# Optimization experiments

Measured on AMD Instinct MI355X. Metric: run time of the kernel, lower is better.

The kernel has to match this reference:

```python
import jax, jax.numpy as jnp
import numpy as np

# physical constants from init_kwargs
N_ACT = 10.0                      # adaptive_activation_n (same for all layers)
MU1, MU2 = 1.0, 10.0
SIGMA = 24.5
G = 0.98
RHO1, RHO2 = 100.0, 1000.0
U_REF, L_REF = 1.0, 0.5
RHO_REF = RHO2
EPS = 2.220446049250313e-16       # np.finfo(float).eps used in abs_interface_grad
ONE_WE = SIGMA / (RHO_REF * U_REF ** 2 * L_REF)
ONE_FR = G * L_REF / U_REF ** 2
RE_DEN = RHO_REF * U_REF * L_REF


def setup_inputs() -> dict:
    key = jax.random.key(0)
    ks = jax.random.split(key, 8)
    N, H, NL = 32768, 250, 7

    def glorot(k, shape):
        fan_in, fan_out = shape[-2], shape[-1]
        s = jnp.sqrt(2.0 / (fan_in + fan_out)).astype(jnp.float32)
        return jax.random.normal(k, shape, dtype=jnp.float32) * s

    return {
        "x": jax.random.normal(ks[0], (N, 1), dtype=jnp.float32),
        "y": jax.random.normal(ks[1], (N, 1), dtype=jnp.float32),
        "t": jax.random.uniform(ks[2], (N, 1), dtype=jnp.float32),
        "W_in": glorot(ks[3], (3, H)),
        "b_in": jnp.zeros((H,), jnp.float32),
        "W_h": glorot(ks[4], (NL - 1, H, H)),
        "b_h": jnp.zeros((NL - 1, H), jnp.float32),
        "W_out": glorot(ks[5], (H, 4)),   # 4 heads: u, v, p, a
        "b_out": jnp.zeros((4,), jnp.float32),
        "act_coeff": jnp.full((NL,), 0.1, jnp.float32),  # adaptive activation coeffs
    }


def _mlp(pt, W_in, b_in, W_h, b_h, W_out, b_out, act_coeff):
    # pt: (3,) -> (4,) outputs [u, v, p=exp(z), a=sigmoid(z)]
    h = jnp.tanh(N_ACT * act_coeff[0] * (pt @ W_in + b_in))
    for i in range(W_h.shape[0]):  # structural loop over 6 hidden layers
        h = jnp.tanh(N_ACT * act_coeff[i + 1] * (h @ W_h[i] + b_h[i]))
    z = h @ W_out + b_out
    return jnp.stack([z[0], z[1], jnp.exp(z[2]), jax.nn.sigmoid(z[3])])


def _pde_residuals(x, y, t, W_in, b_in, W_h, b_h, W_out, b_out, act_coeff):
    pts = jnp.concatenate([x, y, t], axis=1)  # (N, 3)
    f = lambda p: _mlp(p, W_in, b_in, W_h, b_h, W_out, b_out, act_coeff)
    vals = jax.vmap(f)(pts)                              # (N, 4)
    jac = jax.vmap(jax.jacfwd(f))(pts)                   # (N, 4, 3)
    hess = jax.vmap(jax.jacfwd(jax.jacfwd(f)))(pts)      # (N, 4, 3, 3)

    u, v, a = vals[:, 0], vals[:, 1], vals[:, 3]
    u_x, u_y, u_t = jac[:, 0, 0], jac[:, 0, 1], jac[:, 0, 2]
    v_x, v_y, v_t = jac[:, 1, 0], jac[:, 1, 1], jac[:, 1, 2]
    p_x, p_y = jac[:, 2, 0], jac[:, 2, 1]
    a_x, a_y, a_t = jac[:, 3, 0], jac[:, 3, 1], jac[:, 3, 2]
    u_xx, u_yy = hess[:, 0, 0, 0], hess[:, 0, 1, 1]
    v_xx, v_yy = hess[:, 1, 0, 0], hess[:, 1, 1, 1]
    a_xx, a_yy, a_xy = hess[:, 3, 0, 0], hess[:, 3, 1, 1], hess[:, 3, 0, 1]

    mu = MU2 + (MU1 - MU2) * a
    mu_x = (MU1 - MU2) * a_x
    mu_y = (MU1 - MU2) * a_y
    rho = RHO2 + (RHO1 - RHO2) * a

    g = jnp.sqrt(a_x ** 2 + a_y ** 2 + EPS)
    curvature = -((a_xx + a_yy) / g
                  - (a_x ** 2 * a_xx + a_y ** 2 * a_yy + 2.0 * a_x * a_y * a_xy) / (g ** 3))

    one_Re = mu / RE_DEN
    one_Re_x = mu_x / RE_DEN
    one_Re_y = mu_y / RE_DEN

    PDE_m = u_x + v_y
    PDE_a = a_t + u * a_x + v * a_y
    PDE_u = ((u_t + u * u_x + v * u_y) * rho / RHO_REF + p_x
             - ONE_WE * curvature * a_x - one_Re * (u_xx + u_yy)
             - 2.0 * one_Re_x * u_x - one_Re_y * (u_y + v_x))
    PDE_v = ((v_t + u * v_x + v * v_y) * rho / RHO_REF + p_y
             - ONE_WE * curvature * a_y - one_Re * (v_xx + v_yy)
             - rho / RHO_REF * ONE_FR
             - 2.0 * one_Re_y * v_y - one_Re_x * (u_y + v_x))
    return jnp.stack([PDE_m, PDE_u, PDE_v, PDE_a], axis=1)  # (N, 4)


def reference(x, y, t, W_in, b_in, W_h, b_h, W_out, b_out, act_coeff):
    r = _pde_residuals(x, y, t, W_in, b_in, W_h, b_h, W_out, b_out, act_coeff)
    # match PDE_caller's tuple of (N,1) residuals
    return (r[:, 0:1], r[:, 1:2], r[:, 2:3], r[:, 3:4])
```

## Files before the change

kernel.cpp:

```cpp
#include <hip/hip_runtime.h>
#include <math.h>
#include <stdint.h>

#define HP 256
#define PTS 16
#define ROWS 128
#define PSTR 264
#define NLAYER 6
#define WT_ELEMS (6*256*256)
#define PREP_TILES 96

typedef _Float16 half8 __attribute__((ext_vector_type(8)));
typedef _Float16 half2v __attribute__((ext_vector_type(2)));
typedef float  float16v __attribute__((ext_vector_type(16)));

#define C_WI 0
#define C_BI 768
#define C_BH 1024
#define C_WO 2560
#define C_TOT 3584

__device__ __forceinline__ float fast_tanh(float x) {
    float e = __expf(2.0f * x);
    return 1.0f - __fdividef(2.0f, e + 1.0f);
}

__device__ __forceinline__ float16v zero16() {
    float16v z;
    #pragma unroll
    for (int i = 0; i < 16; ++i) z[i] = 0.0f;
    return z;
}

__device__ __forceinline__ int arow(int P, int c) {
    return 32*(P >> 2) + 16*((P >> 1) & 1) + 4*(P & 1) + 8*(c >> 2) + (c & 3);
}

#define MFMA16(A,B,Cc) __builtin_amdgcn_mfma_f32_32x32x16_f16((A),(B),(Cc),0,0,0)

__global__ void prep_kernel(const float* __restrict__ W_in, const float* __restrict__ b_in,
                            const float* __restrict__ W_h,  const float* __restrict__ b_h,
                            const float* __restrict__ W_out, void* __restrict__ wsv)
{
    _Float16* wt = (_Float16*)wsv;
    float* cf = (float*)((char*)wsv + (size_t)WT_ELEMS * 2);
    _Float16* cfh = (_Float16*)(cf + C_TOT);

    const int tid = threadIdx.x;
    const int bid = blockIdx.x;

    if (bid < PREP_TILES) {
        __shared__ _Float16 tile[64 * 65];
        int l  = bid / 16;
        int ka = (bid % 16) >> 2;
        int na = bid & 3;
        int k0 = 64 * ka, n0 = 64 * na;
        #pragma unroll
        for (int pass = 0; pass < 16; ++pass) {
            int idx = pass * 256 + tid;
            int kl = idx >> 6, nl = idx & 63;
            int k = k0 + kl, n = n0 + nl;
            float v = (k < 250 && n < 250) ? W_h[(l*250 + k)*250 + n] : 0.0f;
            tile[kl * 65 + nl] = (_Float16)v;
        }
        __syncthreads();
        #pragma unroll
        for (int b = 0; b < 2; ++b) {
            int slot = tid * 2 + b;
            int lo5  = slot & 31;
            int st_l = (slot >> 5) & 1;
            int hi5  = (slot >> 6) & 1;
            int s_l  = slot >> 7;
            int nl = st_l * 32 + lo5;
            half8 hv;
            #pragma unroll
            for (int j = 0; j < 8; ++j)
                hv[j] = tile[(s_l * 16 + hi5 * 8 + j) * 65 + nl];
            int s    = ka * 4 + s_l;
            int st   = na * 2 + st_l;
            int lane = hi5 * 32 + lo5;
            size_t dst = ((size_t)l << 16) | (s << 12) | (st << 9) | (lane << 3);
            *(half8*)(wt + dst) = hv;
        }
    } else {
        int i0 = (bid - PREP_TILES) * blockDim.x + tid;
        int stride = 8 * blockDim.x;
        for (int i = i0; i < C_TOT; i += stride) {
            float v = 0.0f;
            if (i < C_BI) { int r = i >> 8, j = i & 255; if (j < 250) v = W_in[r*250 + j]; }
            else if (i < C_BH) { int j = i - C_BI; if (j < 250) v = b_in[j]; }
            else if (i < C_WO) { int idx = i - C_BH; int l = idx >> 8, j = idx & 255; if (j < 250) v = b_h[l*250 + j]; }
            else { int idx = i - C_WO; int k = idx >> 2, o = idx & 3; if (k < 250) v = W_out[k*4 + o]; }
            cf[i] = v;
        }
        for (int i = i0; i < 1024; i += stride) {
            int o = i >> 8, k = i & 255;
            cfh[i] = (_Float16)(k < 250 ? W_out[k*4 + o] : 0.0f);
        }
    }
}

__launch_bounds__(512, 4)
__global__ void pinn_mfma(const float* __restrict__ xg, const float* __restrict__ yg,
                          const float* __restrict__ tg, const void* __restrict__ wsv,
                          const float* __restrict__ b_out, const float* __restrict__ act,
                          float* __restrict__ out, int N)
{
    __shared__ _Float16 Ah[ROWS * PSTR];
    __shared__ float zo[PTS][28];

    const _Float16* __restrict__ wt = (const _Float16*)wsv;
    const float* __restrict__ cf = (const float*)((const char*)wsv + (size_t)WT_ELEMS * 2);
    const _Float16* __restrict__ cfh = (const _Float16*)(cf + C_TOT);

    if (blockIdx.x & 1) {
        __builtin_amdgcn_s_sleep(32);
        __builtin_amdgcn_s_sleep(32);
        __builtin_amdgcn_s_sleep(32);
        __builtin_amdgcn_s_sleep(32);
    }

    const int tid  = threadIdx.x;
    const int lane = tid & 63;
    const int w    = tid >> 6;
    const int lo5  = lane & 31;
    const int hi5  = lane >> 5;
    const int n0   = 32*w + lo5;

    {
        int j   = tid & 255;
        int hf  = tid >> 8;
        float wi0 = cf[C_WI + j], wi1 = cf[C_WI + 256 + j], wi2 = cf[C_WI + 512 + j];
        float biv = cf[C_BI + j];
        float c0 = 10.0f * act[0];
        #pragma unroll
        for (int p8 = 0; p8 < 8; ++p8) {
            int p  = 8*hf + p8;
            int gp = blockIdx.x * PTS + p;
            gp = gp < N ? gp : N - 1;
            float px = xg[gp], py = yg[gp], pt = tg[gp];
            float z = px*wi0 + py*wi1 + pt*wi2 + biv;
            float y = fast_tanh(c0 * z);
            float s = 1.0f - y*y;
            float cs = c0 * s;
            float m2 = -2.0f * c0 * cs * y;
            float o[8];
            o[0] = y;           o[1] = cs*wi0;      o[2] = cs*wi1;      o[3] = cs*wi2;
            o[4] = m2*wi0*wi0;  o[5] = m2*wi1*wi1;  o[6] = m2*wi0*wi1;  o[7] = 0.0f;
            #pragma unroll
            for (int c = 0; c < 8; ++c)
                Ah[arow(p, c)*PSTR + j] = (_Float16)o[c];
        }
    }

    for (int L = 0; L < NLAYER; ++L) {
        float cc = 10.0f * act[L + 1];
        const _Float16* __restrict__ ph = wt + ((size_t)L << 16) + ((size_t)w << 9)
                                             + (size_t)lane * 8;

        half8 Bq[4];
        #pragma unroll
        for (int i = 0; i < 4; ++i)
            Bq[i] = *(const half8*)(ph + 4096*i);

        float16v m[4];
        #pragma unroll
        for (int rt = 0; rt < 4; ++rt) m[rt] = zero16();

        __syncthreads();

        const int abase = lo5 * PSTR + 8*hi5;
        half8 a0[4], a1[4];
        #pragma unroll
        for (int rt = 0; rt < 4; ++rt) {
            a0[rt] = *(const half8*)&Ah[abase + 32*rt*PSTR];
            a1[rt] = *(const half8*)&Ah[abase + 32*rt*PSTR + 16];
        }

        #pragma unroll
        for (int s = 0; s < 16; ++s) {
            half8 b = Bq[s & 3];
            if (s < 12)
                Bq[s & 3] = *(const half8*)(ph + 4096*(s + 4));
            half8 cur[4];
            #pragma unroll
            for (int rt = 0; rt < 4; ++rt) { cur[rt] = a0[rt]; a0[rt] = a1[rt]; }
            if (s < 14) {
                #pragma unroll
                for (int rt = 0; rt < 4; ++rt)
                    a1[rt] = *(const half8*)&Ah[abase + 32*rt*PSTR + 16*(s + 2)];
            }
            #pragma unroll
            for (int rt = 0; rt < 4; ++rt)
                m[rt] = MFMA16(cur[rt], b, m[rt]);
        }

        __syncthreads();

        float bb = cf[C_BH + (L << 8) + n0];

        #pragma unroll
        for (int rt = 0; rt < 4; ++rt) {
            float16v mv = m[rt];
            #pragma unroll
            for (int pp = 0; pp < 2; ++pp) {
                float z   = mv[8*pp+0] + bb;
                float zx  = mv[8*pp+1];
                float zy  = mv[8*pp+2];
                float zt  = mv[8*pp+3];
                float zxx = mv[8*pp+4];
                float zyy = mv[8*pp+5];
                float zxy = mv[8*pp+6];
                float y   = fast_tanh(cc * z);
                float sh  = 1.0f - y*y;
                float cs  = cc * sh;
                float m2c = -2.0f * cc * cs * y;
                int r0 = (32*rt + 16*pp + 4*hi5) * PSTR + n0;
                Ah[r0 + 0*PSTR] = (_Float16)y;
                Ah[r0 + 1*PSTR] = (_Float16)(cs*zx);
                Ah[r0 + 2*PSTR] = (_Float16)(cs*zy);
                Ah[r0 + 3*PSTR] = (_Float16)(cs*zt);
                int r1 = r0 + 8*PSTR;
                Ah[r1 + 0*PSTR] = (_Float16)(cs*zxx + m2c*zx*zx);
                Ah[r1 + 1*PSTR] = (_Float16)(cs*zyy + m2c*zy*zy);
                Ah[r1 + 2*PSTR] = (_Float16)(cs*zxy + m2c*zx*zy);
                Ah[r1 + 3*PSTR] = (_Float16)0.0f;
            }
        }
    }

    __syncthreads();
    if (tid < PTS * 28) {
        int p = tid / 28, idx = tid % 28;
        int c = idx >> 2, o = idx & 3;
        const _Float16* rh = &Ah[arow(p, c) * PSTR];
        const _Float16* wo = cfh + (o << 8);
        float s = 0.0f;
        for (int kq = 0; kq < HP/8; ++kq) {
            half8 h  = *(const half8*)(rh + 8*kq);
            half8 ww = *(const half8*)(wo + 8*kq);
#if __has_builtin(__builtin_amdgcn_fdot2)
            #pragma unroll
            for (int j = 0; j < 4; ++j) {
                half2v ha = { h[2*j], h[2*j+1] };
                half2v wa = { ww[2*j], ww[2*j+1] };
                s = __builtin_amdgcn_fdot2(ha, wa, s, false);
            }
#else
            #pragma unroll
            for (int j = 0; j < 8; ++j) s += (float)h[j] * (float)ww[j];
#endif
        }
        zo[p][idx] = s;
    }
    __syncthreads();

    if (tid < PTS) {
        int gp = blockIdx.x * PTS + tid;
        if (gp < N) {
            float zc[7][4];
            #pragma unroll
            for (int c = 0; c < 7; ++c)
                #pragma unroll
                for (int o = 0; o < 4; ++o)
                    zc[c][o] = zo[tid][c*4 + o] + (c == 0 ? b_out[o] : 0.0f);

            float u  = zc[0][0], vv = zc[0][1];
            float u_x = zc[1][0], u_y = zc[2][0], u_t = zc[3][0];
            float u_xx = zc[4][0], u_yy = zc[5][0];
            float v_x = zc[1][1], v_y = zc[2][1], v_t = zc[3][1];
            float v_xx = zc[4][1], v_yy = zc[5][1];

            float ep  = expf(zc[0][2]);
            float p_x = ep * zc[1][2], p_y = ep * zc[2][2];

            float a   = 1.0f / (1.0f + expf(-zc[0][3]));
            float sp  = a * (1.0f - a);
            float spp = sp * (1.0f - 2.0f*a);
            float z1a = zc[1][3], z2a = zc[2][3];
            float a_x = sp * z1a, a_y = sp * z2a, a_t = sp * zc[3][3];
            float a_xx = spp*z1a*z1a + sp*zc[4][3];
            float a_yy = spp*z2a*z2a + sp*zc[5][3];
            float a_xy = spp*z1a*z2a + sp*zc[6][3];

            float mu_x = -9.0f*a_x, mu_y = -9.0f*a_y;
            float mu   = 10.0f - 9.0f*a;
            float rr   = 1.0f - 0.9f*a;
            float g  = sqrtf(a_x*a_x + a_y*a_y + 2.220446049250313e-16f);
            float g3 = g*g*g;
            float curv = -((a_xx + a_yy)/g
                         - (a_x*a_x*a_xx + a_y*a_y*a_yy + 2.0f*a_x*a_y*a_xy)/g3);
            float one_Re   = mu   * 0.002f;
            float one_Re_x = mu_x * 0.002f;
            float one_Re_y = mu_y * 0.002f;

            float PDE_m = u_x + v_y;
            float PDE_a = a_t + u*a_x + vv*a_y;
            float PDE_u = (u_t + u*u_x + vv*u_y)*rr + p_x - 0.049f*curv*a_x
                        - one_Re*(u_xx + u_yy) - 2.0f*one_Re_x*u_x - one_Re_y*(u_y + v_x);
            float PDE_v = (v_t + u*v_x + vv*v_y)*rr + p_y - 0.049f*curv*a_y
                        - one_Re*(v_xx + v_yy) - rr*0.49f
                        - 2.0f*one_Re_y*v_y - one_Re_x*(u_y + v_x);

            out[0*N + gp] = PDE_m;
            out[1*N + gp] = PDE_u;
            out[2*N + gp] = PDE_v;
            out[3*N + gp] = PDE_a;
        }
    }
}

extern "C" void kernel_launch(void* const* d_in, const int* in_sizes, int n_in,
                              void* d_out, int out_size, void* d_ws, size_t ws_size,
                              hipStream_t stream)
{
    const float* x     = (const float*)d_in[0];
    const float* y     = (const float*)d_in[1];
    const float* t     = (const float*)d_in[2];
    const float* W_in  = (const float*)d_in[3];
    const float* b_in  = (const float*)d_in[4];
    const float* W_h   = (const float*)d_in[5];
    const float* b_h   = (const float*)d_in[6];
    const float* W_out = (const float*)d_in[7];
    const float* b_out = (const float*)d_in[8];
    const float* act   = (const float*)d_in[9];
    float* out = (float*)d_out;
    int N = in_sizes[0];

    hipLaunchKernelGGL(prep_kernel, dim3(PREP_TILES + 8), dim3(256), 0, stream,
                       W_in, b_in, W_h, b_h, W_out, d_ws);
    int nb = (N + PTS - 1) / PTS;
    hipLaunchKernelGGL(pinn_mfma, dim3(nb), dim3(512), 0, stream,
                       x, y, t, d_ws, b_out, act, out, N);
}
```

Measured before the change: 335.8 us.

## Ping-pong two point groups to overlap MFMA with tanh epilogue

Each block now processes two 16-point groups in separate LDS buffers. The layer loop is software-pipelined so the MFMA matmul for one group runs interleaved with the tanh/derivative epilogue of the other, hiding epilogue latency behind matrix work. LDS use doubles, so occupancy is lowered to 2 blocks per CU via launch bounds, and the stagger sleep for odd blocks is removed. Register pressure rises from holding two sets of accumulators.

After: 343.7 us. 2.4% more time.

```diff
diff --git a/kernel.cpp b/kernel.cpp
--- a/kernel.cpp
+++ b/kernel.cpp
@@ -3,7 +3,7 @@
 #include <stdint.h>
 
 #define HP 256
-#define PTS 16
+#define PTS 32
 #define ROWS 128
 #define PSTR 264
 #define NLAYER 6
@@ -100,25 +100,85 @@
     }
 }
 
-__launch_bounds__(512, 4)
+#define PHASE(DOK, KPL, LK, KM, DOE, EPL, LE, EM) do {                          \
+  const _Float16* ph_ = wt;                                                      \
+  half8 Bq_[4], a0_[4], a1_[4];                                                  \
+  if (DOK) {                                                                     \
+    ph_ = wt + (((size_t)(LK)) << 16) + ((size_t)w << 9) + (size_t)lane * 8;     \
+    _Pragma("unroll") for (int i_ = 0; i_ < 4; ++i_)                             \
+      Bq_[i_] = *(const half8*)(ph_ + 4096*i_);                                  \
+    _Pragma("unroll") for (int rt_ = 0; rt_ < 4; ++rt_) {                        \
+      KM[rt_] = zero16();                                                        \
+      a0_[rt_] = *(const half8*)&KPL[abase + 32*rt_*PSTR];                       \
+      a1_[rt_] = *(const half8*)&KPL[abase + 32*rt_*PSTR + 16];                  \
+    }                                                                            \
+  }                                                                              \
+  float cc_ = 0.f, bb_ = 0.f;                                                    \
+  if (DOE) {                                                                     \
+    cc_ = 10.0f * act[(LE) + 1];                                                 \
+    bb_ = cf[C_BH + ((LE) << 8) + n0];                                           \
+  }                                                                              \
+  _Pragma("unroll")                                                              \
+  for (int ch_ = 0; ch_ < 8; ++ch_) {                                            \
+    if (DOK) {                                                                   \
+      _Pragma("unroll")                                                          \
+      for (int u_ = 0; u_ < 2; ++u_) {                                           \
+        const int s_ = 2*ch_ + u_;                                               \
+        half8 b_ = Bq_[s_ & 3];                                                  \
+        if (s_ < 12) Bq_[s_ & 3] = *(const half8*)(ph_ + 4096*(s_ + 4));         \
+        half8 cur_[4];                                                           \
+        _Pragma("unroll") for (int rt_ = 0; rt_ < 4; ++rt_) {                    \
+          cur_[rt_] = a0_[rt_]; a0_[rt_] = a1_[rt_];                             \
+        }                                                                        \
+        if (s_ < 14) {                                                           \
+          _Pragma("unroll") for (int rt_ = 0; rt_ < 4; ++rt_)                    \
+            a1_[rt_] = *(const half8*)&KPL[abase + 32*rt_*PSTR + 16*(s_ + 2)];   \
+        }                                                                        \
+        _Pragma("unroll") for (int rt_ = 0; rt_ < 4; ++rt_)                      \
+          KM[rt_] = MFMA16(cur_[rt_], b_, KM[rt_]);                              \
+      }                                                                          \
+    }                                                                            \
+    if (DOE) {                                                                   \
+      const int rt_ = ch_ >> 1, pp_ = ch_ & 1;                                   \
+      float16v mv_ = EM[rt_];                                                    \
+      float z_   = mv_[8*pp_+0] + bb_;                                           \
+      float zx_  = mv_[8*pp_+1];                                                 \
+      float zy_  = mv_[8*pp_+2];                                                 \
+      float zt_  = mv_[8*pp_+3];                                                 \
+      float zxx_ = mv_[8*pp_+4];                                                 \
+      float zyy_ = mv_[8*pp_+5];                                                 \
+      float zxy_ = mv_[8*pp_+6];                                                 \
+      float y_   = fast_tanh(cc_ * z_);                                          \
+      float sh_  = 1.0f - y_*y_;                                                 \
+      float cs_  = cc_ * sh_;                                                    \
+      float m2_  = -2.0f * cc_ * cs_ * y_;                                       \
+      int r0_ = (32*rt_ + 16*pp_ + 4*hi5) * PSTR + n0;                           \
+      EPL[r0_ + 0*PSTR] = (_Float16)y_;                                          \
+      EPL[r0_ + 1*PSTR] = (_Float16)(cs_*zx_);                                   \
+      EPL[r0_ + 2*PSTR] = (_Float16)(cs_*zy_);                                   \
+      EPL[r0_ + 3*PSTR] = (_Float16)(cs_*zt_);                                   \
+      int r1_ = r0_ + 8*PSTR;                                                    \
+      EPL[r1_ + 0*PSTR] = (_Float16)(cs_*zxx_ + m2_*zx_*zx_);                    \
+      EPL[r1_ + 1*PSTR] = (_Float16)(cs_*zyy_ + m2_*zy_*zy_);                    \
+      EPL[r1_ + 2*PSTR] = (_Float16)(cs_*zxy_ + m2_*zx_*zy_);                    \
+      EPL[r1_ + 3*PSTR] = (_Float16)0.0f;                                        \
+    }                                                                            \
+  }                                                                              \
+} while (0)
+
+__launch_bounds__(512, 2)
 __global__ void pinn_mfma(const float* __restrict__ xg, const float* __restrict__ yg,
                           const float* __restrict__ tg, const void* __restrict__ wsv,
                           const float* __restrict__ b_out, const float* __restrict__ act,
                           float* __restrict__ out, int N)
 {
-    __shared__ _Float16 Ah[ROWS * PSTR];
+    __shared__ _Float16 AhA[ROWS * PSTR];
+    __shared__ _Float16 AhB[ROWS * PSTR];
     __shared__ float zo[PTS][28];
 
     const _Float16* __restrict__ wt = (const _Float16*)wsv;
     const float* __restrict__ cf = (const float*)((const char*)wsv + (size_t)WT_ELEMS * 2);
     const _Float16* __restrict__ cfh = (const _Float16*)(cf + C_TOT);
-
-    if (blockIdx.x & 1) {
-        __builtin_amdgcn_s_sleep(32);
-        __builtin_amdgcn_s_sleep(32);
-        __builtin_amdgcn_s_sleep(32);
-        __builtin_amdgcn_s_sleep(32);
-    }
 
     const int tid  = threadIdx.x;
     const int lane = tid & 63;
@@ -126,17 +186,18 @@
     const int lo5  = lane & 31;
     const int hi5  = lane >> 5;
     const int n0   = 32*w + lo5;
+    const int abase = lo5 * PSTR + 8*hi5;
 
     {
-        int j   = tid & 255;
-        int hf  = tid >> 8;
+        int j  = tid & 255;
+        int hf = tid >> 8;
+        _Float16* pl = hf ? AhB : AhA;
         float wi0 = cf[C_WI + j], wi1 = cf[C_WI + 256 + j], wi2 = cf[C_WI + 512 + j];
         float biv = cf[C_BI + j];
         float c0 = 10.0f * act[0];
         #pragma unroll
-        for (int p8 = 0; p8 < 8; ++p8) {
-            int p  = 8*hf + p8;
-            int gp = blockIdx.x * PTS + p;
+        for (int p = 0; p < 16; ++p) {
+            int gp = blockIdx.x * PTS + 16*hf + p;
             gp = gp < N ? gp : N - 1;
             float px = xg[gp], py = yg[gp], pt = tg[gp];
             float z = px*wi0 + py*wi1 + pt*wi2 + biv;
@@ -149,91 +210,32 @@
             o[4] = m2*wi0*wi0;  o[5] = m2*wi1*wi1;  o[6] = m2*wi0*wi1;  o[7] = 0.0f;
             #pragma unroll
             for (int c = 0; c < 8; ++c)
-                Ah[arow(p, c)*PSTR + j] = (_Float16)o[c];
-        }
-    }
+                pl[arow(p, c)*PSTR + j] = (_Float16)o[c];
+        }
+    }
+
+    float16v mA[4], mB[4];
+
+    __syncthreads();
+    PHASE(1, AhA, 0, mA,  0, AhA, 0, mA);
+    __syncthreads();
 
     for (int L = 0; L < NLAYER; ++L) {
-        float cc = 10.0f * act[L + 1];
-        const _Float16* __restrict__ ph = wt + ((size_t)L << 16) + ((size_t)w << 9)
-                                             + (size_t)lane * 8;
-
-        half8 Bq[4];
-        #pragma unroll
-        for (int i = 0; i < 4; ++i)
-            Bq[i] = *(const half8*)(ph + 4096*i);
-
-        float16v m[4];
-        #pragma unroll
-        for (int rt = 0; rt < 4; ++rt) m[rt] = zero16();
-
+        PHASE(1, AhB, L, mB,  1, AhA, L, mA);
         __syncthreads();
-
-        const int abase = lo5 * PSTR + 8*hi5;
-        half8 a0[4], a1[4];
-        #pragma unroll
-        for (int rt = 0; rt < 4; ++rt) {
-            a0[rt] = *(const half8*)&Ah[abase + 32*rt*PSTR];
-            a1[rt] = *(const half8*)&Ah[abase + 32*rt*PSTR + 16];
-        }
-
-        #pragma unroll
-        for (int s = 0; s < 16; ++s) {
-            half8 b = Bq[s & 3];
-            if (s < 12)
-                Bq[s & 3] = *(const half8*)(ph + 4096*(s + 4));
-            half8 cur[4];
-            #pragma unroll
-            for (int rt = 0; rt < 4; ++rt) { cur[rt] = a0[rt]; a0[rt] = a1[rt]; }
-            if (s < 14) {
-                #pragma unroll
-                for (int rt = 0; rt < 4; ++rt)
-                    a1[rt] = *(const half8*)&Ah[abase + 32*rt*PSTR + 16*(s + 2)];
-            }
-            #pragma unroll
-            for (int rt = 0; rt < 4; ++rt)
-                m[rt] = MFMA16(cur[rt], b, m[rt]);
-        }
-
+        if (L + 1 < NLAYER) {
+            PHASE(1, AhA, L+1, mA,  1, AhB, L, mB);
+        } else {
+            PHASE(0, AhA, 0, mA,  1, AhB, L, mB);
+        }
         __syncthreads();
-
-        float bb = cf[C_BH + (L << 8) + n0];
-
-        #pragma unroll
-        for (int rt = 0; rt < 4; ++rt) {
-            float16v mv = m[rt];
-            #pragma unroll
-            for (int pp = 0; pp < 2; ++pp) {
-                float z   = mv[8*pp+0] + bb;
-                float zx  = mv[8*pp+1];
-                float zy  = mv[8*pp+2];
-                float zt  = mv[8*pp+3];
-                float zxx = mv[8*pp+4];
-                float zyy = mv[8*pp+5];
-                float zxy = mv[8*pp+6];
-                float y   = fast_tanh(cc * z);
-                float sh  = 1.0f - y*y;
-                float cs  = cc * sh;
-                float m2c = -2.0f * cc * cs * y;
-                int r0 = (32*rt + 16*pp + 4*hi5) * PSTR + n0;
-                Ah[r0 + 0*PSTR] = (_Float16)y;
-                Ah[r0 + 1*PSTR] = (_Float16)(cs*zx);
-                Ah[r0 + 2*PSTR] = (_Float16)(cs*zy);
-                Ah[r0 + 3*PSTR] = (_Float16)(cs*zt);
-                int r1 = r0 + 8*PSTR;
-                Ah[r1 + 0*PSTR] = (_Float16)(cs*zxx + m2c*zx*zx);
-                Ah[r1 + 1*PSTR] = (_Float16)(cs*zyy + m2c*zy*zy);
-                Ah[r1 + 2*PSTR] = (_Float16)(cs*zxy + m2c*zx*zy);
-                Ah[r1 + 3*PSTR] = (_Float16)0.0f;
-            }
-        }
-    }
-
-    __syncthreads();
-    if (tid < PTS * 28) {
-        int p = tid / 28, idx = tid % 28;
+    }
+
+    for (int job = tid; job < PTS * 28; job += 512) {
+        int p = job / 28, idx = job % 28;
         int c = idx >> 2, o = idx & 3;
-        const _Float16* rh = &Ah[arow(p, c) * PSTR];
+        const _Float16* pl = (p < 16) ? AhA : AhB;
+        const _Float16* rh = &pl[arow(p & 15, c) * PSTR];
         const _Float16* wo = cfh + (o << 8);
         float s = 0.0f;
         for (int kq = 0; kq < HP/8; ++kq) {
```
